# Performance work log

Hardware: AMD Instinct MI355X
Metric: run time of the kernel (lower is better)

The kernel has to match this reference:

```python
import jax, jax.numpy as jnp
import numpy as np

C, D, H, Z, B = 10, 3072, 512, 256, 2048  # classes, img_dim, hidden, latent, batch


def setup_inputs() -> dict:
    key = jax.random.key(0)
    ks = jax.random.split(key, 8)
    def w(k, shape, fan_in):
        return jax.random.normal(k, shape, jnp.float32) * (1.0 / np.sqrt(fan_in)).astype(np.float32)
    return {
        "img": jax.random.normal(ks[0], (B, D), jnp.float32),
        "label": jax.random.randint(ks[1], (B,), 0, C, dtype=jnp.int32),
        "enc_w1": w(ks[2], (C, D, H), D), "enc_b1": jnp.zeros((C, H), jnp.float32),
        "enc_w2": w(ks[3], (C, H, Z), H), "enc_b2": jnp.zeros((C, Z), jnp.float32),
        "dec_w1": w(ks[4], (C, Z, H), Z), "dec_b1": jnp.zeros((C, H), jnp.float32),
        "dec_w2": w(ks[5], (C, H, D), H), "dec_b2": jnp.zeros((C, D), jnp.float32),
    }


def reference(img, label, enc_w1, enc_b1, enc_w2, enc_b2,
              dec_w1, dec_b1, dec_w2, dec_b2):
    # Label-conditioned dispatch: rows with label==c go through expert c's
    # encoder-decoder; outputs scattered back into a zero-initialized image.
    # Loop is over a small fixed class count (structurally distinct experts);
    # masked-select via jnp.where is mathematically identical to the
    # gather/scatter in the torch code (absent classes contribute nothing).
    out_img = jnp.zeros_like(img)
    n_classes = enc_w1.shape[0]
    for c in range(n_classes):
        h = jax.nn.relu(img @ enc_w1[c] + enc_b1[c])       # [B,H]
        z = h @ enc_w2[c] + enc_b2[c]                      # [B,Z] latent code
        h2 = jax.nn.relu(z @ dec_w1[c] + dec_b1[c])        # [B,H]
        y = h2 @ dec_w2[c] + dec_b2[c]                     # [B,D]
        out_img = jnp.where((label == c)[:, None], y, out_img)
    loss = jnp.mean((out_img - img) ** 2)
    return loss, out_img
```

## Files before the change

### kernel.cpp

```cpp
#include <hip/hip_runtime.h>
#include <hip/hip_bf16.h>

#define C_CLS 10
#define DIM   3072
#define HID   512
#define LAT   256
#define BATCH 2048
#define BM    64
#define GRID_TILES 42

typedef __attribute__((ext_vector_type(8))) short  s16x8;
typedef __attribute__((ext_vector_type(4))) float  f32x4;
typedef __attribute__((ext_vector_type(8))) __bf16 bf16x8;

struct Meta {
    int offsets[C_CLS + 1];
    int ntiles;
    int tileClass[GRID_TILES];
    int tileRow[GRID_TILES];
    int perm[BATCH];
};

__device__ __forceinline__ unsigned short f2bf(float f) {
    unsigned u = __builtin_bit_cast(unsigned, f);
    unsigned r = (u + 0x7fffu + ((u >> 16) & 1u)) >> 16;
    return (unsigned short)r;
}

__device__ __forceinline__ f32x4 mfma16(s16x8 a, s16x8 b, f32x4 c) {
    return __builtin_amdgcn_mfma_f32_16x16x32_bf16(
        __builtin_bit_cast(bf16x8, a), __builtin_bit_cast(bf16x8, b), c, 0, 0, 0);
}

__global__ __launch_bounds__(256) void setup_kernel(const int* __restrict__ label,
                                                    Meta* __restrict__ mt,
                                                    float* __restrict__ out) {
    __shared__ int h[C_CLS];
    __shared__ int loff[C_CLS + 1];
    int tid = threadIdx.x;
    if (tid < C_CLS) h[tid] = 0;
    __syncthreads();
    for (int i = tid; i < BATCH; i += 256) atomicAdd(&h[label[i]], 1);
    __syncthreads();
    if (tid == 0) {
        int s = 0, nt = 0;
        for (int c = 0; c < C_CLS; ++c) { loff[c] = s; s += h[c]; }
        loff[C_CLS] = s;
        for (int c = 0; c < C_CLS; ++c) {
            mt->offsets[c] = loff[c];
            int cnt = h[c];
            for (int t = 0; t < cnt; t += BM) {
                mt->tileClass[nt] = c;
                mt->tileRow[nt]   = loff[c] + t;
                ++nt;
            }
            h[c] = loff[c];
        }
        mt->offsets[C_CLS] = loff[C_CLS];
        mt->ntiles = nt;
        out[0] = 0.0f;
    }
    __syncthreads();
    for (int i = tid; i < BATCH; i += 256) {
        int pos = atomicAdd(&h[label[i]], 1);
        mt->perm[pos] = i;
    }
}

template <int K, int N, bool RELU, bool FINAL, bool GATHER>
__global__ __launch_bounds__(256) void gemm_kernel(const void* __restrict__ Ain,
                                                   const float* __restrict__ W,
                                                   const float* __restrict__ bias,
                                                   unsigned short* __restrict__ Aout,
                                                   float* __restrict__ outF,
                                                   const float* __restrict__ img,
                                                   const Meta* __restrict__ mt) {
    int ty = blockIdx.y;
    if (ty >= mt->ntiles) return;
    const int c    = mt->tileClass[ty];
    const int r0   = mt->tileRow[ty];
    const int rend = mt->offsets[c + 1];
    const int n0   = blockIdx.x * 64;

    const float* Wc = W + (size_t)c * K * N + n0;

    __shared__ __align__(16) unsigned short As[2][64 * 64];
    __shared__ __align__(16) unsigned short Bs[2][64 * 64];

    const int tid  = threadIdx.x;
    const int lane = tid & 63;
    const int wid  = tid >> 6;
    const int wm   = wid >> 1, wn = wid & 1;

    const int aRow0 = tid >> 3;
    const int aSlot = tid & 7;
    const int bO    = tid >> 5;
    const int bN2   = tid & 31;

    float4 ga[4];
    s16x8  aa[2];
    float2 bb[8];

    auto load_tile = [&](int k0) {
#pragma unroll
        for (int h = 0; h < 2; ++h) {
            int row = aRow0 + h * 32;
            int ar  = min(r0 + row, rend - 1);
            if constexpr (GATHER) {
                int orig = mt->perm[ar];
                const float* src = (const float*)Ain + (size_t)orig * K + k0 + aSlot * 8;
                ga[2 * h]     = *(const float4*)(src);
                ga[2 * h + 1] = *(const float4*)(src + 4);
            } else {
                aa[h] = *(const s16x8*)((const unsigned short*)Ain + (size_t)ar * K + k0 + aSlot * 8);
            }
        }
        const float* src = Wc + (size_t)(k0 + 8 * bO) * N + 2 * bN2;
#pragma unroll
        for (int i = 0; i < 8; ++i) bb[i] = *(const float2*)(src + (size_t)i * N);
    };

    auto write_tile = [&](int buf) {
#pragma unroll
        for (int h = 0; h < 2; ++h) {
            int row = aRow0 + h * 32;
            s16x8 v;
            if constexpr (GATHER) {
#pragma unroll
                for (int j = 0; j < 4; ++j) {
                    ((unsigned short*)&v)[j]     = f2bf(((const float*)&ga[2 * h])[j]);
                    ((unsigned short*)&v)[4 + j] = f2bf(((const float*)&ga[2 * h + 1])[j]);
                }
            } else {
                v = aa[h];
            }
            *(s16x8*)(&As[buf][row * 64 + ((aSlot ^ (row & 7))) * 8]) = v;
        }
#pragma unroll
        for (int nn = 0; nn < 2; ++nn) {
            int n = 2 * bN2 + nn;
            s16x8 v;
#pragma unroll
            for (int i = 0; i < 8; ++i)
                ((unsigned short*)&v)[i] = f2bf(nn ? bb[i].y : bb[i].x);
            *(s16x8*)(&Bs[buf][n * 64 + ((bO ^ (n & 7))) * 8]) = v;
        }
    };

    f32x4 acc[2][2] = {};
    constexpr int NT = K / 64;

    load_tile(0);
    write_tile(0);
    __syncthreads();

    for (int t = 0; t < NT; ++t) {
        int cur = t & 1;
        if (t + 1 < NT) load_tile((t + 1) * 64);
#pragma unroll
        for (int ks = 0; ks < 2; ++ks) {
            int kslot = ks * 4 + (lane >> 4);
            int rA0 = wm * 32 + (lane & 15), rA1 = rA0 + 16;
            int rB0 = wn * 32 + (lane & 15), rB1 = rB0 + 16;
            s16x8 a0 = *(const s16x8*)(&As[cur][rA0 * 64 + (kslot ^ (rA0 & 7)) * 8]);
            s16x8 a1 = *(const s16x8*)(&As[cur][rA1 * 64 + (kslot ^ (rA1 & 7)) * 8]);
            s16x8 b0 = *(const s16x8*)(&Bs[cur][rB0 * 64 + (kslot ^ (rB0 & 7)) * 8]);
            s16x8 b1 = *(const s16x8*)(&Bs[cur][rB1 * 64 + (kslot ^ (rB1 & 7)) * 8]);
            acc[0][0] = mfma16(a0, b0, acc[0][0]);
            acc[0][1] = mfma16(a0, b1, acc[0][1]);
            acc[1][0] = mfma16(a1, b0, acc[1][0]);
            acc[1][1] = mfma16(a1, b1, acc[1][1]);
        }
        if (t + 1 < NT) write_tile(cur ^ 1);
        __syncthreads();
    }

    const int col = lane & 15;
    const int rq  = lane >> 4;
    if constexpr (!FINAL) {
#pragma unroll
        for (int mi = 0; mi < 2; ++mi)
#pragma unroll
            for (int ni = 0; ni < 2; ++ni) {
                int n    = n0 + wn * 32 + ni * 16 + col;
                float bv = bias[(size_t)c * N + n];
#pragma unroll
                for (int r = 0; r < 4; ++r) {
                    int m = r0 + wm * 32 + mi * 16 + rq * 4 + r;
                    if (m < rend) {
                        float v = acc[mi][ni][r] + bv;
                        if (RELU) v = fmaxf(v, 0.0f);
                        Aout[(size_t)m * N + n] = f2bf(v);
                    }
                }
            }
    } else {
        float lsum = 0.0f;
#pragma unroll
        for (int mi = 0; mi < 2; ++mi) {
#pragma unroll
            for (int r = 0; r < 4; ++r) {
                int m = r0 + wm * 32 + mi * 16 + rq * 4 + r;
                if (m < rend) {
                    int orig = mt->perm[m];
#pragma unroll
                    for (int ni = 0; ni < 2; ++ni) {
                        int n   = n0 + wn * 32 + ni * 16 + col;
                        float v = acc[mi][ni][r] + bias[(size_t)c * N + n];
                        size_t idx = (size_t)orig * N + n;
                        outF[1 + idx] = v;
                        float d = v - img[idx];
                        lsum += d * d;
                    }
                }
            }
        }
#pragma unroll
        for (int o = 32; o > 0; o >>= 1) lsum += __shfl_down(lsum, o);
        __shared__ float red[4];
        if (lane == 0) red[wid] = lsum;
        __syncthreads();
        if (tid == 0)
            atomicAdd(&outF[0],
                      (red[0] + red[1] + red[2] + red[3]) * (1.0f / ((float)BATCH * (float)DIM)));
    }
}

extern "C" void kernel_launch(void* const* d_in, const int* in_sizes, int n_in,
                              void* d_out, int out_size, void* d_ws, size_t ws_size,
                              hipStream_t stream) {
    const float* img    = (const float*)d_in[0];
    const int*   label  = (const int*)d_in[1];
    const float* enc_w1 = (const float*)d_in[2];
    const float* enc_b1 = (const float*)d_in[3];
    const float* enc_w2 = (const float*)d_in[4];
    const float* enc_b2 = (const float*)d_in[5];
    const float* dec_w1 = (const float*)d_in[6];
    const float* dec_b1 = (const float*)d_in[7];
    const float* dec_w2 = (const float*)d_in[8];
    const float* dec_b2 = (const float*)d_in[9];
    float* out = (float*)d_out;

    auto alignup = [](size_t x) { return (x + 255) & ~(size_t)255; };
    char* p = (char*)d_ws;
    size_t off = 0;
    Meta* meta = (Meta*)p;                            off += alignup(sizeof(Meta));
    unsigned short* H1 = (unsigned short*)(p + off);  off += alignup((size_t)BATCH * HID * 2);
    unsigned short* Z1 = (unsigned short*)(p + off);  off += alignup((size_t)BATCH * LAT * 2);
    unsigned short* H2 = (unsigned short*)(p + off);  off += alignup((size_t)BATCH * HID * 2);
    (void)ws_size; (void)in_sizes; (void)n_in; (void)out_size;

    setup_kernel<<<1, 256, 0, stream>>>(label, meta, out);

    gemm_kernel<DIM, HID, true,  false, true ><<<dim3(HID / 64, GRID_TILES), 256, 0, stream>>>(
        img, enc_w1, enc_b1, H1, nullptr, nullptr, meta);
    gemm_kernel<HID, LAT, false, false, false><<<dim3(LAT / 64, GRID_TILES), 256, 0, stream>>>(
        H1, enc_w2, enc_b2, Z1, nullptr, nullptr, meta);
    gemm_kernel<LAT, HID, true,  false, false><<<dim3(HID / 64, GRID_TILES), 256, 0, stream>>>(
        Z1, dec_w1, dec_b1, H2, nullptr, nullptr, meta);
    gemm_kernel<HID, DIM, false, true,  false><<<dim3(DIM / 64, GRID_TILES), 256, 0, stream>>>(
        H2, dec_w2, dec_b2, nullptr, out, img, meta);
}
```

Before: 296.4 us.

## Split-K the GEMM chain, reducing fp32 partials in the next layer's load

Adds split-K along a grid z dimension to the first three GEMMs, which raises the block count on the small-N layers (for example 4x42 blocks for the encoder's first layer). Each split writes fp32 partial sums to workspace. The next layer's A-tile load sums those partials, adds the bias and applies ReLU before converting to bf16, so no separate reduction kernel is needed. The cost is more intermediate traffic, since activations are now fp32 and multiplied by the number of partials, and redundant partial reads in every N-column block.

New measurement: 303.6 us. 1.02x slower.

```diff
diff --git a/kernel.cpp b/kernel.cpp
--- a/kernel.cpp
+++ b/kernel.cpp
@@ -67,22 +67,25 @@
     }
 }
 
-template <int K, int N, bool RELU, bool FINAL, bool GATHER>
-__global__ __launch_bounds__(256) void gemm_kernel(const void* __restrict__ Ain,
+template <int KTOT, int KSPLIT, int N, int NPART, bool RELUIN, bool FINAL>
+__global__ __launch_bounds__(256) void gemm_kernel(const float* __restrict__ Ain,
+                                                   const float* __restrict__ abias,
                                                    const float* __restrict__ W,
-                                                   const float* __restrict__ bias,
-                                                   unsigned short* __restrict__ Aout,
+                                                   const float* __restrict__ obias,
+                                                   float* __restrict__ Pout,
                                                    float* __restrict__ outF,
                                                    const float* __restrict__ img,
                                                    const Meta* __restrict__ mt) {
     int ty = blockIdx.y;
     if (ty >= mt->ntiles) return;
-    const int c    = mt->tileClass[ty];
-    const int r0   = mt->tileRow[ty];
-    const int rend = mt->offsets[c + 1];
-    const int n0   = blockIdx.x * 64;
-
-    const float* Wc = W + (size_t)c * K * N + n0;
+    const int c     = mt->tileClass[ty];
+    const int r0    = mt->tileRow[ty];
+    const int rend  = mt->offsets[c + 1];
+    const int n0    = blockIdx.x * 64;
+    const int kbase = blockIdx.z * (KTOT / KSPLIT);
+    constexpr int NT = KTOT / KSPLIT / 64;
+
+    const float* Wc = W + (size_t)c * KTOT * N + n0;
 
     __shared__ __align__(16) unsigned short As[2][64 * 64];
     __shared__ __align__(16) unsigned short Bs[2][64 * 64];
@@ -97,8 +100,9 @@
     const int bO    = tid >> 5;
     const int bN2   = tid & 31;
 
-    float4 ga[4];
-    s16x8  aa[2];
+    constexpr int NP = (NPART == 0) ? 1 : NPART;
+    float4 ga[NP][2][2];
+    float4 gbias[2];
     float2 bb[8];
 
     auto load_tile = [&](int k0) {
@@ -106,14 +110,24 @@
         for (int h = 0; h < 2; ++h) {
             int row = aRow0 + h * 32;
             int ar  = min(r0 + row, rend - 1);
-            if constexpr (GATHER) {
+            if constexpr (NPART == 0) {
                 int orig = mt->perm[ar];
-                const float* src = (const float*)Ain + (size_t)orig * K + k0 + aSlot * 8;
-                ga[2 * h]     = *(const float4*)(src);
-                ga[2 * h + 1] = *(const float4*)(src + 4);
+                const float* src = Ain + (size_t)orig * KTOT + k0 + aSlot * 8;
+                ga[0][h][0] = *(const float4*)(src);
+                ga[0][h][1] = *(const float4*)(src + 4);
             } else {
-                aa[h] = *(const s16x8*)((const unsigned short*)Ain + (size_t)ar * K + k0 + aSlot * 8);
-            }
+#pragma unroll
+                for (int p = 0; p < NP; ++p) {
+                    const float* src = Ain + ((size_t)p * BATCH + ar) * KTOT + k0 + aSlot * 8;
+                    ga[p][h][0] = *(const float4*)(src);
+                    ga[p][h][1] = *(const float4*)(src + 4);
+                }
+            }
+        }
+        if constexpr (NPART > 0) {
+            const float* bsrc = abias + (size_t)c * KTOT + k0 + aSlot * 8;
+            gbias[0] = *(const float4*)(bsrc);
+            gbias[1] = *(const float4*)(bsrc + 4);
         }
         const float* src = Wc + (size_t)(k0 + 8 * bO) * N + 2 * bN2;
 #pragma unroll
@@ -125,15 +139,21 @@
         for (int h = 0; h < 2; ++h) {
             int row = aRow0 + h * 32;
             s16x8 v;
-            if constexpr (GATHER) {
+#pragma unroll
+            for (int q = 0; q < 2; ++q)
 #pragma unroll
                 for (int j = 0; j < 4; ++j) {
-                    ((unsigned short*)&v)[j]     = f2bf(((const float*)&ga[2 * h])[j]);
-                    ((unsigned short*)&v)[4 + j] = f2bf(((const float*)&ga[2 * h + 1])[j]);
-                }
-            } else {
-                v = aa[h];
-            }
+                    float s;
+                    if constexpr (NPART == 0) {
+                        s = ((const float*)&ga[0][h][q])[j];
+                    } else {
+                        s = ((const float*)&gbias[q])[j];
+#pragma unroll
+                        for (int p = 0; p < NP; ++p) s += ((const float*)&ga[p][h][q])[j];
+                        if (RELUIN) s = fmaxf(s, 0.0f);
+                    }
+                    ((unsigned short*)&v)[q * 4 + j] = f2bf(s);
+                }
             *(s16x8*)(&As[buf][row * 64 + ((aSlot ^ (row & 7))) * 8]) = v;
         }
 #pragma unroll
@@ -148,15 +168,14 @@
     };
 
     f32x4 acc[2][2] = {};
-    constexpr int NT = K / 64;
-
-    load_tile(0);
+
+    load_tile(kbase);
     write_tile(0);
     __syncthreads();
 
     for (int t = 0; t < NT; ++t) {
         int cur = t & 1;
-        if (t + 1 < NT) load_tile((t + 1) * 64);
+        if (t + 1 < NT) load_tile(kbase + (t + 1) * 64);
 #pragma unroll
         for (int ks = 0; ks < 2; ++ks) {
             int kslot = ks * 4 + (lane >> 4);
@@ -178,20 +197,16 @@
     const int col = lane & 15;
     const int rq  = lane >> 4;
     if constexpr (!FINAL) {
+        float* P = Pout + (size_t)blockIdx.z * BATCH * N;
 #pragma unroll
         for (int mi = 0; mi < 2; ++mi)
 #pragma unroll
             for (int ni = 0; ni < 2; ++ni) {
-                int n    = n0 + wn * 32 + ni * 16 + col;
-                float bv = bias[(size_t)c * N + n];
+                int n = n0 + wn * 32 + ni * 16 + col;
 #pragma unroll
                 for (int r = 0; r < 4; ++r) {
                     int m = r0 + wm * 32 + mi * 16 + rq * 4 + r;
-                    if (m < rend) {
-                        float v = acc[mi][ni][r] + bv;
-                        if (RELU) v = fmaxf(v, 0.0f);
-                        Aout[(size_t)m * N + n] = f2bf(v);
-                    }
+                    if (m < rend) P[(size_t)m * N + n] = acc[mi][ni][r];
                 }
             }
     } else {
@@ -206,7 +221,7 @@
 #pragma unroll
                     for (int ni = 0; ni < 2; ++ni) {
                         int n   = n0 + wn * 32 + ni * 16 + col;
-                        float v = acc[mi][ni][r] + bias[(size_t)c * N + n];
+                        float v = acc[mi][ni][r] + obias[(size_t)c * N + n];
                         size_t idx = (size_t)orig * N + n;
                         outF[1 + idx] = v;
                         float d = v - img[idx];
@@ -244,20 +259,20 @@
     auto alignup = [](size_t x) { return (x + 255) & ~(size_t)255; };
     char* p = (char*)d_ws;
     size_t off = 0;
-    Meta* meta = (Meta*)p;                            off += alignup(sizeof(Meta));
-    unsigned short* H1 = (unsigned short*)(p + off);  off += alignup((size_t)BATCH * HID * 2);
-    unsigned short* Z1 = (unsigned short*)(p + off);  off += alignup((size_t)BATCH * LAT * 2);
-    unsigned short* H2 = (unsigned short*)(p + off);  off += alignup((size_t)BATCH * HID * 2);
+    Meta* meta = (Meta*)p;                  off += alignup(sizeof(Meta));
+    float* P1  = (float*)(p + off);         off += alignup((size_t)4 * BATCH * HID * 4);
+    float* PZ  = (float*)(p + off);         off += alignup((size_t)4 * BATCH * LAT * 4);
+    float* PH2 = (float*)(p + off);         off += alignup((size_t)2 * BATCH * HID * 4);
     (void)ws_size; (void)in_sizes; (void)n_in; (void)out_size;
 
     setup_kernel<<<1, 256, 0, stream>>>(label, meta, out);
 
-    gemm_kernel<DIM, HID, true,  false, true ><<<dim3(HID / 64, GRID_TILES), 256, 0, stream>>>(
-        img, enc_w1, enc_b1, H1, nullptr, nullptr, meta);
-    gemm_kernel<HID, LAT, false, false, false><<<dim3(LAT / 64, GRID_TILES), 256, 0, stream>>>(
-        H1, enc_w2, enc_b2, Z1, nullptr, nullptr, meta);
-    gemm_kernel<LAT, HID, true,  false, false><<<dim3(HID / 64, GRID_TILES), 256, 0, stream>>>(
-        Z1, dec_w1, dec_b1, H2, nullptr, nullptr, meta);
-    gemm_kernel<HID, DIM, false, true,  false><<<dim3(DIM / 64, GRID_TILES), 256, 0, stream>>>(
-        H2, dec_w2, dec_b2, nullptr, out, img, meta);
-}
+    gemm_kernel<DIM, 4, HID, 0, false, false><<<dim3(HID / 64, GRID_TILES, 4), 256, 0, stream>>>(
+        img, nullptr, enc_w1, nullptr, P1, nullptr, nullptr, meta);
+    gemm_kernel<HID, 4, LAT, 4, true, false><<<dim3(LAT / 64, GRID_TILES, 4), 256, 0, stream>>>(
+        P1, enc_b1, enc_w2, nullptr, PZ, nullptr, nullptr, meta);
+    gemm_kernel<LAT, 2, HID, 4, false, false><<<dim3(HID / 64, GRID_TILES, 2), 256, 0, stream>>>(
+        PZ, enc_b2, dec_w1, nullptr, PH2, nullptr, nullptr, meta);
+    gemm_kernel<HID, 1, DIM, 2, true, true><<<dim3(DIM / 64, GRID_TILES, 1), 256, 0, stream>>>(
+        PH2, dec_b1, dec_w2, dec_b2, nullptr, out, img, meta);
+}
```
